# Optimization experiments

Measured on AMD Instinct MI355X. Metric: run time of the kernel, lower is better.

Reference implementation:

```python
import jax, jax.numpy as jnp
import numpy as np

NHEAD = 8
LAYER_NAMES = ('self', 'cross', 'self', 'cross')
EPS = 1e-6


def ln(x, g, b, eps=1e-5):
    m = jnp.mean(x, -1, keepdims=True)
    v = jnp.mean((x - m) ** 2, -1, keepdims=True)
    return (x - m) * jax.lax.rsqrt(v + eps) * g + b


def linear_attention(q, k, v, q_mask, kv_mask):
    # q: [N, L, H, D], k/v: [N, S, H, D]; LoFTR LinearAttention (elu+1 feature map)
    Q = jax.nn.elu(q) + 1.0
    K = jax.nn.elu(k) + 1.0
    if q_mask is not None:
        Q = Q * q_mask[:, :, None, None].astype(Q.dtype)
    if kv_mask is not None:
        mk = kv_mask[:, :, None, None].astype(K.dtype)
        K = K * mk
        v = v * mk
    v_len = v.shape[1]
    v = v / v_len
    KV = jnp.einsum('nshd,nshv->nhdv', K, v)
    Z = 1.0 / (jnp.einsum('nlhd,nhd->nlh', Q, K.sum(1)) + EPS)
    return jnp.einsum('nlhd,nhdv,nlh->nlhv', Q, KV, Z) * v_len


def enc_layer(x, src, q_mask, kv_mask, Wq, Wk, Wv, Wm, W1, W2, g1, b1, g2, b2):
    # x: [N, L, C], src: [N, S, C]
    N, L, C = x.shape
    S = src.shape[1]
    H, D = NHEAD, C // NHEAD
    q = (x @ Wq).reshape(N, L, H, D)
    k = (src @ Wk).reshape(N, S, H, D)
    v = (src @ Wv).reshape(N, S, H, D)
    msg = linear_attention(q, k, v, q_mask, kv_mask).reshape(N, L, C)
    msg = ln(msg @ Wm, g1, b1)
    msg = ln(jnp.tanh(jnp.concatenate([x, msg], axis=-1) @ W1) @ W2, g2, b2)
    return x + msg


def sample_descriptors(kp, fmap, s):
    # kp: [B, L, K, 2] (x, y) raw-image pixel coords; fmap: [B, C, H, W]; s: stride
    B, C, H, W = fmap.shape
    k = kp - s / 2 + 0.5
    denom = jnp.array([W * s - s / 2 - 0.5, H * s - s / 2 - 0.5], dtype=kp.dtype)
    k = (k / denom) * 2.0 - 1.0  # normalized [-1, 1]
    px = (k[..., 0] + 1.0) * 0.5 * (W - 1)  # align_corners=True grid_sample
    py = (k[..., 1] + 1.0) * 0.5 * (H - 1)
    x0 = jnp.floor(px)
    y0 = jnp.floor(py)
    wx = (px - x0)[..., None]
    wy = (py - y0)[..., None]
    x0i = jnp.clip(x0, 0, W - 1).astype(jnp.int32)
    x1i = jnp.clip(x0 + 1, 0, W - 1).astype(jnp.int32)
    y0i = jnp.clip(y0, 0, H - 1).astype(jnp.int32)
    y1i = jnp.clip(y0 + 1, 0, H - 1).astype(jnp.int32)
    fm = jnp.transpose(fmap, (0, 2, 3, 1))  # [B, H, W, C]
    bidx = jnp.arange(B)[:, None, None]
    g00 = fm[bidx, y0i, x0i]
    g01 = fm[bidx, y0i, x1i]
    g10 = fm[bidx, y1i, x0i]
    g11 = fm[bidx, y1i, x1i]
    out = (1 - wy) * ((1 - wx) * g00 + wx * g01) + wy * ((1 - wx) * g10 + wx * g11)
    # SuperPoint-style L2 normalization of sampled descriptors
    out = out / (jnp.linalg.norm(out, axis=-1, keepdims=True) + 1e-8)
    return out  # [B, L, K, C]


def geo_transformer(feat0, feat1, kp0_cross, kp1_cross, mask_self0, mask_self1,
                    mask_cross0, mask_cross1, Wq, Wk, Wv, Wm, W1, W2, g1, b1, g2, b2,
                    h0, w0, h1, w1, scale):
    B, L0, C = feat0.shape
    L1 = feat1.shape[1]
    K = kp0_cross.shape[2]
    for i, name in enumerate(LAYER_NAMES):
        p = (Wq[i], Wk[i], Wv[i], Wm[i], W1[i], W2[i], g1[i], b1[i], g2[i], b2[i])
        if name == 'self':
            # source = masked subset of x == full source with kv-mask (v_length cancels)
            feat0 = enc_layer(feat0, feat0, None, mask_self0, *p)
            feat1 = enc_layer(feat1, feat1, None, mask_self1, *p)
        else:
            fmap0 = jnp.transpose(feat0.reshape(B, h0, w0, C), (0, 3, 1, 2))
            fmap1 = jnp.transpose(feat1.reshape(B, h1, w1, C), (0, 3, 1, 2))
            f0c = sample_descriptors(kp0_cross, fmap0, scale)  # [B, L1, K, C]
            f1c = sample_descriptors(kp1_cross, fmap1, scale)  # [B, L0, K, C]
            x0 = feat0.reshape(B * L0, 1, C)
            x1 = feat1.reshape(B * L1, 1, C)
            nf0 = enc_layer(x0, f1c.reshape(B * L0, K, C), None,
                            mask_cross1.reshape(B * L0, K), *p)
            nf1 = enc_layer(x1, f0c.reshape(B * L1, K, C), None,
                            mask_cross0.reshape(B * L1, K), *p)
            feat0 = nf0.reshape(B, L0, C)
            feat1 = nf1.reshape(B, L1, C)
    return feat0, feat1


def setup_inputs() -> dict:
    key = jax.random.key(0)
    B, H0, W0, C, K, S, NL = 2, 64, 64, 256, 9, 8, 4
    L = H0 * W0
    ks = jax.random.split(key, 16)
    std = (2.0 / (C + C)) ** 0.5
    std2 = (2.0 / (2 * C + 2 * C)) ** 0.5
    std3 = (2.0 / (2 * C + C)) ** 0.5
    kp0 = jnp.stack([
        jax.random.uniform(ks[2], (B, L, K)) * (W0 * S),
        jax.random.uniform(ks[3], (B, L, K)) * (H0 * S)], axis=-1)
    kp1 = jnp.stack([
        jax.random.uniform(ks[4], (B, L, K)) * (W0 * S),
        jax.random.uniform(ks[5], (B, L, K)) * (H0 * S)], axis=-1)
    return {
        'feat0': jax.random.normal(ks[0], (B, L, C), jnp.float32),
        'feat1': jax.random.normal(ks[1], (B, L, C), jnp.float32),
        'kp0_cross': kp0.astype(jnp.float32),
        'kp1_cross': kp1.astype(jnp.float32),
        'mask_self0': jax.random.bernoulli(ks[6], 0.9, (B, L)),
        'mask_self1': jax.random.bernoulli(ks[7], 0.9, (B, L)),
        'mask_cross0': jax.random.bernoulli(ks[8], 0.8, (B, L, K)),
        'mask_cross1': jax.random.bernoulli(ks[9], 0.8, (B, L, K)),
        'Wq': jax.random.normal(ks[10], (NL, C, C), jnp.float32) * std,
        'Wk': jax.random.normal(ks[11], (NL, C, C), jnp.float32) * std,
        'Wv': jax.random.normal(ks[12], (NL, C, C), jnp.float32) * std,
        'Wm': jax.random.normal(ks[13], (NL, C, C), jnp.float32) * std,
        'W1': jax.random.normal(ks[14], (NL, 2 * C, 2 * C), jnp.float32) * std2,
        'W2': jax.random.normal(ks[15], (NL, 2 * C, C), jnp.float32) * std3,
        'g1': jnp.ones((NL, C), jnp.float32),
        'b1': jnp.zeros((NL, C), jnp.float32),
        'g2': jnp.ones((NL, C), jnp.float32),
        'b2': jnp.zeros((NL, C), jnp.float32),
        'h0': H0, 'w0': W0, 'h1': H0, 'w1': W0, 'scale': S,
    }


def reference(feat0, feat1, kp0_cross, kp1_cross, mask_self0, mask_self1,
              mask_cross0, mask_cross1, Wq, Wk, Wv, Wm, W1, W2, g1, b1, g2, b2,
              h0, w0, h1, w1, scale):
    return geo_transformer(feat0, feat1, kp0_cross, kp1_cross, mask_self0, mask_self1,
                           mask_cross0, mask_cross1, Wq, Wk, Wv, Wm, W1, W2,
                           g1, b1, g2, b2, h0, w0, h1, w1, scale)
```

## Files before the change

kernel.cpp:

```cpp
#include <hip/hip_runtime.h>
#include <cstddef>


#define NROWS 16384

typedef unsigned short ushort_t;
typedef __attribute__((ext_vector_type(8))) short short8;
typedef __attribute__((ext_vector_type(4))) float f32x4;
typedef __attribute__((ext_vector_type(4))) unsigned short ushort4_t;
typedef __attribute__((ext_vector_type(8))) unsigned short ushort8_t;

__device__ __forceinline__ float b2f(unsigned short u) {
    union { unsigned int i; float f; } v; v.i = (unsigned int)u << 16; return v.f;
}
__device__ __forceinline__ unsigned short f2b(float x) {
    union { float f; unsigned int i; } v; v.f = x;
    unsigned int r = v.i + 0x7fffu + ((v.i >> 16) & 1u);
    return (unsigned short)(r >> 16);
}
__device__ __forceinline__ float elu1(float x) {
    return x > 0.f ? x + 1.f : __expf(x);
}

#define ASYNC_COPY16(gptr, lptr) \
    __builtin_amdgcn_global_load_lds((const __attribute__((address_space(1))) void*)(gptr), \
                                     (__attribute__((address_space(3))) void*)(lptr), 16, 0, 0)

__global__ __launch_bounds__(256) void gemm_bf16_kernel(
    const ushort_t* __restrict__ A0, int lda0,
    const ushort_t* __restrict__ Wt, int ldw,
    ushort_t* __restrict__ C, int ldc, int Kd,
    float* __restrict__ zbuf, int znf4)
{
    __shared__ ushort_t As[128 * 64];
    __shared__ ushort_t Bs[128 * 64];

    int tid = threadIdx.x;
    int m0 = blockIdx.y * 128;
    int n0 = blockIdx.x * 128;
    int lane = tid & 63, w = tid >> 6;
    int wrow = w >> 1, wcol = w & 1;
    int quad = lane >> 4, l16 = lane & 15;

    if (zbuf && blockIdx.y == 0) {
        int nblk = gridDim.x;
        for (int i = blockIdx.x * 256 + tid; i < znf4; i += nblk * 256)
            *(float4*)&zbuf[(size_t)i * 4] = (float4){0.f, 0.f, 0.f, 0.f};
    }

    f32x4 acc[4][4];
    #pragma unroll
    for (int i = 0; i < 4; i++)
        #pragma unroll
        for (int j = 0; j < 4; j++) acc[i][j] = (f32x4){0.f, 0.f, 0.f, 0.f};

    for (int kb = 0; kb < Kd; kb += 64) {
        #pragma unroll
        for (int q = 0; q < 4; q++) {
            int s = q * 256 + tid;
            int kk = s >> 9, p = s & 511;
            int row = p >> 2, c4 = p & 3;
            ASYNC_COPY16(A0 + (size_t)(m0 + row) * lda0 + kb + kk * 32 + c4 * 8,
                         (char*)As + s * 16);
        }
        #pragma unroll
        for (int q = 0; q < 4; q++) {
            int s = q * 256 + tid;
            int kk = s >> 9, p = s & 511;
            int row = p >> 2, c4 = p & 3;
            ASYNC_COPY16(Wt + (size_t)(n0 + row) * ldw + kb + kk * 32 + c4 * 8,
                         (char*)Bs + s * 16);
        }
        __syncthreads();

        #pragma unroll
        for (int kk = 0; kk < 2; kk++) {
            short8 af[4], bf[4];
            #pragma unroll
            for (int mt = 0; mt < 4; mt++)
                af[mt] = *(const short8*)&As[kk * 4096 + (wrow * 64 + mt * 16 + l16) * 32 + quad * 8];
            #pragma unroll
            for (int nt = 0; nt < 4; nt++)
                bf[nt] = *(const short8*)&Bs[kk * 4096 + (wcol * 64 + nt * 16 + l16) * 32 + quad * 8];
            #pragma unroll
            for (int mt = 0; mt < 4; mt++)
                #pragma unroll
                for (int nt = 0; nt < 4; nt++)
                    acc[mt][nt] = __builtin_amdgcn_mfma_f32_16x16x32_bf16(
                        af[mt], bf[nt], acc[mt][nt], 0, 0, 0);
        }
        __syncthreads();
    }

    #pragma unroll
    for (int mt = 0; mt < 4; mt++) {
        int row = m0 + wrow * 64 + mt * 16 + quad * 4;
        #pragma unroll
        for (int nt = 0; nt < 4; nt++) {
            int col = n0 + wcol * 64 + nt * 16 + l16;
            #pragma unroll
            for (int r = 0; r < 4; r++)
                C[(size_t)(row + r) * ldc + col] = f2b(acc[mt][nt][r]);
        }
    }
}

__global__ __launch_bounds__(256) void gemm_ln_kernel(
    const ushort_t* __restrict__ A, int lda,
    const ushort_t* __restrict__ Wt, int ldw, int Kd,
    const float* __restrict__ g, const float* __restrict__ bp,
    ushort_t* __restrict__ OutBf)
{
    __shared__ ushort_t As[32 * 64];
    __shared__ ushort_t Bs[256 * 64];
    __shared__ float rsum[4][32];
    __shared__ float rsq[4][32];

    int tid = threadIdx.x;
    int m0 = blockIdx.x * 32;
    int lane = tid & 63, w = tid >> 6;
    int quad = lane >> 4, l16 = lane & 15;

    f32x4 acc[2][4];
    #pragma unroll
    for (int i = 0; i < 2; i++)
        #pragma unroll
        for (int j = 0; j < 4; j++) acc[i][j] = (f32x4){0.f, 0.f, 0.f, 0.f};

    for (int kb = 0; kb < Kd; kb += 64) {
        {
            int s = tid;
            int kk = s >> 7, p = s & 127;
            int row = p >> 2, c4 = p & 3;
            ASYNC_COPY16(A + (size_t)(m0 + row) * lda + kb + kk * 32 + c4 * 8,
                         (char*)As + s * 16);
        }
        #pragma unroll
        for (int q = 0; q < 8; q++) {
            int s = q * 256 + tid;
            int kk = s >> 10, p = s & 1023;
            int row = p >> 2, c4 = p & 3;
            ASYNC_COPY16(Wt + (size_t)(row) * ldw + kb + kk * 32 + c4 * 8,
                         (char*)Bs + s * 16);
        }
        __syncthreads();

        #pragma unroll
        for (int kk = 0; kk < 2; kk++) {
            short8 af[2], bf[4];
            #pragma unroll
            for (int mt = 0; mt < 2; mt++)
                af[mt] = *(const short8*)&As[kk * 1024 + (mt * 16 + l16) * 32 + quad * 8];
            #pragma unroll
            for (int nt = 0; nt < 4; nt++)
                bf[nt] = *(const short8*)&Bs[kk * 8192 + (w * 64 + nt * 16 + l16) * 32 + quad * 8];
            #pragma unroll
            for (int mt = 0; mt < 2; mt++)
                #pragma unroll
                for (int nt = 0; nt < 4; nt++)
                    acc[mt][nt] = __builtin_amdgcn_mfma_f32_16x16x32_bf16(
                        af[mt], bf[nt], acc[mt][nt], 0, 0, 0);
        }
        __syncthreads();
    }

    #pragma unroll
    for (int mt = 0; mt < 2; mt++)
        #pragma unroll
        for (int r = 0; r < 4; r++) {
            float s = 0.f, q = 0.f;
            #pragma unroll
            for (int nt = 0; nt < 4; nt++) {
                float v = acc[mt][nt][r];
                s += v; q += v * v;
            }
            #pragma unroll
            for (int off = 1; off < 16; off <<= 1) {
                s += __shfl_xor(s, off, 64);
                q += __shfl_xor(q, off, 64);
            }
            if (l16 == 0) {
                rsum[w][mt * 16 + quad * 4 + r] = s;
                rsq[w][mt * 16 + quad * 4 + r]  = q;
            }
        }
    __syncthreads();

    #pragma unroll
    for (int mt = 0; mt < 2; mt++) {
        #pragma unroll
        for (int r = 0; r < 4; r++) {
            int rl = mt * 16 + quad * 4 + r;
            float s = rsum[0][rl] + rsum[1][rl] + rsum[2][rl] + rsum[3][rl];
            float q = rsq[0][rl] + rsq[1][rl] + rsq[2][rl] + rsq[3][rl];
            float m = s * (1.f / 256.f);
            float var = q * (1.f / 256.f) - m * m;
            float rs = rsqrtf(var + 1e-5f);
            size_t row = (size_t)(m0 + rl);
            #pragma unroll
            for (int nt = 0; nt < 4; nt++) {
                int col = w * 64 + nt * 16 + l16;
                float y = (acc[mt][nt][r] - m) * rs * g[col] + bp[col];
                OutBf[row * 256 + col] = f2b(y);
            }
        }
    }
}

__global__ __launch_bounds__(256) void mlp_fused_kernel(
    const ushort_t* __restrict__ Xb, const ushort_t* __restrict__ L1,
    const ushort_t* __restrict__ W1t, const ushort_t* __restrict__ W2t,
    const float* __restrict__ g, const float* __restrict__ bp,
    ushort_t* __restrict__ XbfOut, const float* __restrict__ Xin,
    float* __restrict__ Xout)
{
    __shared__ ushort_t Tt[32 * 512];
    __shared__ char buf[20480];

    ushort_t* As  = (ushort_t*)buf;
    ushort_t* Bs  = (ushort_t*)(buf + 4096);
    ushort_t* Bs2 = (ushort_t*)buf;
    float* rsum = (float*)buf;
    float* rsq  = (float*)(buf + 512);

    int tid = threadIdx.x;
    int m0 = blockIdx.x * 32;
    int lane = tid & 63, w = tid >> 6;
    int quad = lane >> 4, l16 = lane & 15;

    for (int np = 0; np < 4; np++) {
        f32x4 acc[2][2];
        #pragma unroll
        for (int i = 0; i < 2; i++)
            #pragma unroll
            for (int j = 0; j < 2; j++) acc[i][j] = (f32x4){0.f, 0.f, 0.f, 0.f};

        for (int kb = 0; kb < 512; kb += 64) {
            const ushort_t* Ab = (kb < 256) ? Xb : L1;
            int kc = (kb < 256) ? kb : kb - 256;
            {
                int s = tid;
                int kk = s >> 7, p = s & 127;
                ASYNC_COPY16(Ab + (size_t)(m0 + (p >> 2)) * 256 + kc + kk * 32 + (p & 3) * 8,
                             (char*)As + s * 16);
            }
            #pragma unroll
            for (int q = 0; q < 4; q++) {
                int s = q * 256 + tid;
                int kk = s >> 9, p = s & 511;
                ASYNC_COPY16(W1t + (size_t)(np * 128 + (p >> 2)) * 512 + kb + kk * 32 + (p & 3) * 8,
                             (char*)Bs + s * 16);
            }
            __syncthreads();

            #pragma unroll
            for (int kk = 0; kk < 2; kk++) {
                short8 af[2], bfr[2];
                #pragma unroll
                for (int mt = 0; mt < 2; mt++)
                    af[mt] = *(const short8*)&As[kk * 1024 + (mt * 16 + l16) * 32 + quad * 8];
                #pragma unroll
                for (int nt = 0; nt < 2; nt++)
                    bfr[nt] = *(const short8*)&Bs[kk * 4096 + (w * 32 + nt * 16 + l16) * 32 + quad * 8];
                #pragma unroll
                for (int mt = 0; mt < 2; mt++)
                    #pragma unroll
                    for (int nt = 0; nt < 2; nt++)
                        acc[mt][nt] = __builtin_amdgcn_mfma_f32_16x16x32_bf16(
                            af[mt], bfr[nt], acc[mt][nt], 0, 0, 0);
            }
            __syncthreads();
        }

        #pragma unroll
        for (int mt = 0; mt < 2; mt++)
            #pragma unroll
            for (int nt = 0; nt < 2; nt++)
                #pragma unroll
                for (int r = 0; r < 4; r++) {
                    int trow = mt * 16 + quad * 4 + r;
                    int col = np * 128 + w * 32 + nt * 16 + l16;
                    int c8s = (col >> 3) ^ (trow & 7);
                    Tt[trow * 512 + c8s * 8 + (col & 7)] = f2b(tanhf(acc[mt][nt][r]));
                }
    }

    f32x4 acc2[2][2][2];
    #pragma unroll
    for (int a = 0; a < 2; a++)
        #pragma unroll
        for (int i = 0; i < 2; i++)
            #pragma unroll
            for (int j = 0; j < 2; j++) acc2[a][i][j] = (f32x4){0.f, 0.f, 0.f, 0.f};

    for (int pass = 0; pass < 2; pass++) {
        for (int kb = 0; kb < 512; kb += 64) {
            #pragma unroll
            for (int q = 0; q < 4; q++) {
                int s = q * 256 + tid;
                int kk = s >> 9, p = s & 511;
                ASYNC_COPY16(W2t + (size_t)(pass * 128 + (p >> 2)) * 512 + kb + kk * 32 + (p & 3) * 8,
                             (char*)Bs2 + s * 16);
            }
            __syncthreads();

            #pragma unroll
            for (int kk = 0; kk < 2; kk++) {
                short8 af[2], bfr[2];
                #pragma unroll
                for (int mt = 0; mt < 2; mt++) {
                    int row = mt * 16 + l16;
                    int blk = ((kb >> 3) + kk * 4 + quad) ^ (row & 7);
                    af[mt] = *(const short8*)&Tt[row * 512 + blk * 8];
                }
                #pragma unroll
                for (int nt = 0; nt < 2; nt++)
                    bfr[nt] = *(const short8*)&Bs2[kk * 4096 + (w * 32 + nt * 16 + l16) * 32 + quad * 8];
                #pragma unroll
                for (int mt = 0; mt < 2; mt++)
                    #pragma unroll
                    for (int nt = 0; nt < 2; nt++)
                        acc2[pass][mt][nt] = __builtin_amdgcn_mfma_f32_16x16x32_bf16(
                            af[mt], bfr[nt], acc2[pass][mt][nt], 0, 0, 0);
            }
            __syncthreads();
        }
    }

    #pragma unroll
    for (int mt = 0; mt < 2; mt++)
        #pragma unroll
        for (int r = 0; r < 4; r++) {
            float s = 0.f, q = 0.f;
            #pragma unroll
            for (int pass = 0; pass < 2; pass++)
                #pragma unroll
                for (int nt = 0; nt < 2; nt++) {
                    float v = acc2[pass][mt][nt][r];
                    s += v; q += v * v;
                }
            #pragma unroll
            for (int off = 1; off < 16; off <<= 1) {
                s += __shfl_xor(s, off, 64);
                q += __shfl_xor(q, off, 64);
            }
            if (l16 == 0) {
                rsum[w * 32 + mt * 16 + quad * 4 + r] = s;
                rsq[w * 32 + mt * 16 + quad * 4 + r]  = q;
            }
        }
    __syncthreads();

    #pragma unroll
    for (int mt = 0; mt < 2; mt++) {
        #pragma unroll
        for (int r = 0; r < 4; r++) {
            int rl = mt * 16 + quad * 4 + r;
            float s = rsum[rl] + rsum[32 + rl] + rsum[64 + rl] + rsum[96 + rl];
            float q = rsq[rl] + rsq[32 + rl] + rsq[64 + rl] + rsq[96 + rl];
            float m = s * (1.f / 256.f);
            float var = q * (1.f / 256.f) - m * m;
            float rs = rsqrtf(var + 1e-5f);
            size_t row = (size_t)(m0 + rl);
            #pragma unroll
            for (int pass = 0; pass < 2; pass++)
                #pragma unroll
                for (int nt = 0; nt < 2; nt++) {
                    int col = pass * 128 + w * 32 + nt * 16 + l16;
                    float y = (acc2[pass][mt][nt][r] - m) * rs * g[col] + bp[col];
                    float xn = Xin[row * 256 + col] + y;
                    Xout[row * 256 + col] = xn;
                    XbfOut[row * 256 + col] = f2b(xn);
                }
        }
    }
}

__global__ __launch_bounds__(256) void wprep_kernel(
    const float* __restrict__ Wq, const float* __restrict__ Wk,
    const float* __restrict__ Wv, const float* __restrict__ Wm,
    const float* __restrict__ W1, const float* __restrict__ W2,
    ushort_t* __restrict__ Wqkvt, ushort_t* __restrict__ Wmt,
    ushort_t* __restrict__ W1t, ushort_t* __restrict__ W2t)
{
    int t = blockIdx.x;
    int layer = t / 640, r = t % 640;
    const float* src; ushort_t* dst;
    int ldsrc, lddst, tn, tk;
    if (r < 192) {
        int grp = r / 64, rr = r % 64; tn = rr / 8; tk = rr % 8;
        src = (grp == 0 ? Wq : grp == 1 ? Wk : Wv) + (size_t)layer * 65536;
        ldsrc = 256;
        dst = Wqkvt + (size_t)layer * 196608 + (size_t)grp * 65536;
        lddst = 256;
    } else if (r < 256) {
        int rr = r - 192; tn = rr / 8; tk = rr % 8;
        src = Wm + (size_t)layer * 65536; ldsrc = 256;
        dst = Wmt + (size_t)layer * 65536; lddst = 256;
    } else if (r < 512) {
        int rr = r - 256; tn = rr / 16; tk = rr % 16;
        src = W1 + (size_t)layer * 262144; ldsrc = 512;
        dst = W1t + (size_t)layer * 262144; lddst = 512;
    } else {
        int rr = r - 512; tn = rr / 16; tk = rr % 16;
        src = W2 + (size_t)layer * 131072; ldsrc = 256;
        dst = W2t + (size_t)layer * 131072; lddst = 512;
    }
    int n0 = tn * 32, k0 = tk * 32;
    __shared__ float tileS[32][33];
    int j = threadIdx.x & 31, i0 = threadIdx.x >> 5;
    #pragma unroll
    for (int p = 0; p < 4; p++) {
        int i = i0 + p * 8;
        tileS[i][j] = src[(size_t)(k0 + i) * ldsrc + n0 + j];
    }
    __syncthreads();
    #pragma unroll
    for (int p = 0; p < 4; p++) {
        int i = i0 + p * 8;
        dst[(size_t)(n0 + i) * lddst + k0 + j] = f2b(tileS[j][i]);
    }
}

__global__ __launch_bounds__(256) void init_kernel(
    const float* __restrict__ f0, const float* __restrict__ f1,
    float* __restrict__ X, ushort_t* __restrict__ Xbf)
{
    int idx = blockIdx.x * 256 + threadIdx.x;
    size_t e = (size_t)idx * 4;
    float4 v = (e < 2097152) ? *(const float4*)&f0[e] : *(const float4*)&f1[e - 2097152];
    *(float4*)&X[e] = v;
    ushort4_t u = { f2b(v.x), f2b(v.y), f2b(v.z), f2b(v.w) };
    *(ushort4_t*)&Xbf[e] = u;
}

__global__ __launch_bounds__(256) void kv_reduce_kernel(
    const ushort_t* __restrict__ QKV,
    const int* __restrict__ mask0, const int* __restrict__ mask1,
    float* __restrict__ KV, float* __restrict__ Ksum)
{
    int g = blockIdx.y;
    int t = g >> 4, b = (g >> 3) & 1, h = g & 7;
    const int* mask = t ? mask1 : mask0;
    int rowbase = t * 8192 + b * 4096;
    int s_begin = blockIdx.x * 256;

    __shared__ float sK[32][32];
    __shared__ float sV[32][32];

    int tid = threadIdx.x;
    int e  = tid & 31;
    int dq = tid >> 5;

    float acc[4] = {0.f, 0.f, 0.f, 0.f};
    float ks[4]  = {0.f, 0.f, 0.f, 0.f};

    for (int s0 = s_begin; s0 < s_begin + 256; s0 += 32) {
        #pragma unroll
        for (int q = 0; q < 2; q++) {
            int idx = tid + q * 256;
            int rl = idx >> 4;
            int part = idx & 15;
            int s = s0 + rl;
            size_t row = (size_t)(rowbase + s);
            float m = mask[b * 4096 + s] ? 1.f : 0.f;
            if (part < 8) {
                ushort4_t u = *(const ushort4_t*)&QKV[row * 768 + 256 + h * 32 + part * 4];
                float4 f = { elu1(b2f(u.x)) * m, elu1(b2f(u.y)) * m,
                             elu1(b2f(u.z)) * m, elu1(b2f(u.w)) * m };
                *(float4*)&sK[rl][part * 4] = f;
            } else {
                ushort4_t u = *(const ushort4_t*)&QKV[row * 768 + 512 + h * 32 + (part - 8) * 4];
                float4 f = { b2f(u.x) * m, b2f(u.y) * m, b2f(u.z) * m, b2f(u.w) * m };
                *(float4*)&sV[rl][(part - 8) * 4] = f;
            }
        }
        __syncthreads();

        #pragma unroll
        for (int s = 0; s < 32; s++) {
            float4 kq = *(const float4*)&sK[s][dq * 4];
            float vv = sV[s][e];
            acc[0] += kq.x * vv;
            acc[1] += kq.y * vv;
            acc[2] += kq.z * vv;
            acc[3] += kq.w * vv;
            ks[0] += kq.x; ks[1] += kq.y; ks[2] += kq.z; ks[3] += kq.w;
        }
        __syncthreads();
    }

    #pragma unroll
    for (int j = 0; j < 4; j++)
        atomicAdd(&KV[(size_t)g * 1024 + (dq * 4 + j) * 32 + e], acc[j]);
    if (e == 0) {
        #pragma unroll
        for (int j = 0; j < 4; j++)
            atomicAdd(&Ksum[g * 32 + dq * 4 + j], ks[j]);
    }
}

__global__ __launch_bounds__(256) void attn_apply_kernel(
    const ushort_t* __restrict__ QKV, const float* __restrict__ KV,
    const float* __restrict__ Ksum, ushort_t* __restrict__ MSG)
{
    int row = blockIdx.x;
    int t = row >> 13, bb = (row >> 12) & 1;
    int gb = (t * 2 + bb) * 8;
    int c = threadIdx.x, h = c >> 5, e = c & 31;
    int g = gb + h;

    __shared__ float sQ[256];
    float qf = elu1(b2f(QKV[(size_t)row * 768 + c]));
    sQ[c] = qf;
    __syncthreads();

    float p = qf * Ksum[g * 32 + e];
    #pragma unroll
    for (int off = 16; off; off >>= 1) p += __shfl_xor(p, off, 32);
    float Z = 1.f / (p + 1e-6f);

    float acc = 0.f;
    #pragma unroll
    for (int d = 0; d < 32; d++)
        acc += sQ[h * 32 + d] * KV[(size_t)g * 1024 + d * 32 + e];

    MSG[(size_t)row * 256 + c] = f2b(acc * Z);
}

__global__ __launch_bounds__(256) void gram_kernel(
    const ushort_t* __restrict__ Xbf, float* __restrict__ Gm)
{
    int a = blockIdx.x * 4 + (threadIdx.x >> 6);
    int lane = threadIdx.x & 63;
    int img = a / 4225;
    int rr = a - img * 4225;
    int ay = rr / 65, ax = rr - ay * 65;
    int xa = ax > 0 ? ax - 1 : 0;
    int xb = ax < 64 ? ax : 63;
    if (ax == 0) xb = 0;
    int ya = ay > 0 ? ay - 1 : 0;
    int yb = ay < 64 ? ay : 63;
    if (ay == 0) yb = 0;

    size_t rbase = (size_t)img * 4096;
    size_t r0 = (rbase + ya * 64 + xa) * 256;
    size_t r1 = (rbase + ya * 64 + xb) * 256;
    size_t r2 = (rbase + yb * 64 + xa) * 256;
    size_t r3 = (rbase + yb * 64 + xb) * 256;

    int c4 = lane * 4;
    ushort4_t u0 = *(const ushort4_t*)&Xbf[r0 + c4];
    ushort4_t u1 = *(const ushort4_t*)&Xbf[r1 + c4];
    ushort4_t u2 = *(const ushort4_t*)&Xbf[r2 + c4];
    ushort4_t u3 = *(const ushort4_t*)&Xbf[r3 + c4];

    float p[10] = {0,0,0,0,0,0,0,0,0,0};
    #pragma unroll
    for (int j = 0; j < 4; j++) {
        float f0 = b2f(u0[j]), f1 = b2f(u1[j]), f2 = b2f(u2[j]), f3 = b2f(u3[j]);
        p[0] += f0 * f0; p[1] += f0 * f1; p[2] += f0 * f2; p[3] += f0 * f3;
        p[4] += f1 * f1; p[5] += f1 * f2; p[6] += f1 * f3;
        p[7] += f2 * f2; p[8] += f2 * f3; p[9] += f3 * f3;
    }
    #pragma unroll
    for (int k = 0; k < 10; k++)
        #pragma unroll
        for (int off = 32; off; off >>= 1) p[k] += __shfl_xor(p[k], off, 64);

    if (lane == 0) {
        #pragma unroll
        for (int k = 0; k < 10; k++) Gm[(size_t)a * 12 + k] = p[k];
    }
}

__global__ __launch_bounds__(256) void cross_fused_kernel(
    const ushort_t* __restrict__ QKV, const float* __restrict__ Gm,
    const float* __restrict__ kp0, const float* __restrict__ kp1,
    const int* __restrict__ maskc0, const int* __restrict__ maskc1,
    ushort_t* __restrict__ MSG)
{
    int wv = threadIdx.x >> 6;
    int lane = threadIdx.x & 63;
    int half = lane >> 5;
    int l32 = lane & 31;

    int blk = blockIdx.x;
    int qd = (blk & 7) >> 1;
    int within = ((blk >> 3) << 1) | (blk & 1);
    int row = qd * 4096 + within * 4 + wv;

    int t = row >> 13;
    int bl = row & 8191;
    int ts = 1 - t;
    const float* kp = ts ? kp1 : kp0;
    const int* mask = (t == 0) ? maskc1 : maskc0;
    int img = ts * 2 + (bl >> 12);
    int rb = img * 4096;
    const float* Gimg = Gm + (size_t)img * 50700;

    int c8 = l32 * 8;

    ushort8_t qu = *(const ushort8_t*)&QKV[(size_t)row * 768 + c8];
    float qf[8];
    #pragma unroll
    for (int j = 0; j < 8; j++) qf[j] = elu1(b2f(qu[j]));

    int sbase[5], sdx[5], sdy[5];
    float su0[5], su1[5], su2[5], su3[5], sm[5];
    #pragma unroll
    for (int si = 0; si < 5; si++) {
        int s9 = half + 2 * si;
        int valid = (s9 < 9);
        int r = bl * 9 + (valid ? s9 : 0);
        sm[si] = (valid && mask[r] != 0) ? 1.f : 0.f;

        float2 xy = *(const float2*)&kp[(size_t)r * 2];
        float px = (xy.x - 3.5f) * (63.f / 507.5f);
        float py = (xy.y - 3.5f) * (63.f / 507.5f);
        float fx = floorf(px), fy = floorf(py);
        float wx = px - fx, wy = py - fy;
        int ix = (int)fx, iy = (int)fy;
        int xa = ix > 0 ? ix : 0;
        int xb = ix + 1 > 0 ? (ix + 1 < 63 ? ix + 1 : 63) : 0;
        int ya = iy > 0 ? iy : 0;
        int yb = iy + 1 > 0 ? (iy + 1 < 63 ? iy + 1 : 63) : 0;

        float w0 = (1.f - wy) * (1.f - wx);
        float w1 = (1.f - wy) * wx;
        float w2 = wy * (1.f - wx);
        float w3 = wy * wx;

        const float* G = &Gimg[(size_t)((iy + 1) * 65 + (ix + 1)) * 12];
        float4 ga = *(const float4*)&G[0];
        float4 gb4 = *(const float4*)&G[4];
        float2 gc = *(const float2*)&G[8];
        float ss = w0 * w0 * ga.x + w1 * w1 * gb4.x + w2 * w2 * gb4.w + w3 * w3 * gc.y
                 + 2.f * (w0 * w1 * ga.y + w0 * w2 * ga.z + w0 * w3 * ga.w
                        + w1 * w2 * gb4.y + w1 * w3 * gb4.z + w2 * w3 * gc.x);
        float inv = 1.f / (sqrtf(ss) + 1e-8f);
        su0[si] = w0 * inv; su1[si] = w1 * inv;
        su2[si] = w2 * inv; su3[si] = w3 * inv;

        sbase[si] = (rb + ya * 64 + xa) * 768;
        sdx[si] = (xb - xa) * 768;
        sdy[si] = (yb - ya) * 49152;
    }

    ushort8_t kR[2][4], vR[2][4];

#define LOADKV(bufi, si_) do { \
        size_t bK = (size_t)sbase[si_] + 256 + c8; \
        size_t bV = (size_t)sbase[si_] + 512 + c8; \
        int dx = sdx[si_], dy = sdy[si_]; \
        kR[bufi][0] = *(const ushort8_t*)&QKV[bK]; \
        kR[bufi][1] = *(const ushort8_t*)&QKV[bK + dx]; \
        kR[bufi][2] = *(const ushort8_t*)&QKV[bK + dy]; \
        kR[bufi][3] = *(const ushort8_t*)&QKV[bK + dx + dy]; \
        vR[bufi][0] = *(const ushort8_t*)&QKV[bV]; \
        vR[bufi][1] = *(const ushort8_t*)&QKV[bV + dx]; \
        vR[bufi][2] = *(const ushort8_t*)&QKV[bV + dy]; \
        vR[bufi][3] = *(const ushort8_t*)&QKV[bV + dx + dy]; \
    } while (0)

    float zsum = 0.f;
    float acc[8] = {0, 0, 0, 0, 0, 0, 0, 0};

    LOADKV(0, 0);
    #pragma unroll
    for (int si = 0; si < 5; si++) {
        int cur = si & 1;
        if (si + 1 < 5) {
            if (cur == 0) LOADKV(1, si + 1);
            else          LOADKV(0, si + 1);
        }
        float u0 = su0[si], u1 = su1[si], u2 = su2[si], u3 = su3[si];
        float vc[8];
        float p = 0.f;
        #pragma unroll
        for (int j = 0; j < 8; j++) {
            float kc = u0 * b2f(kR[cur][0][j]) + u1 * b2f(kR[cur][1][j])
                     + u2 * b2f(kR[cur][2][j]) + u3 * b2f(kR[cur][3][j]);
            vc[j] = u0 * b2f(vR[cur][0][j]) + u1 * b2f(vR[cur][1][j])
                  + u2 * b2f(vR[cur][2][j]) + u3 * b2f(vR[cur][3][j]);
            p += qf[j] * elu1(kc);
        }
        p += __shfl_xor(p, 1, 64);
        p += __shfl_xor(p, 2, 64);
        p *= sm[si];

        zsum += p;
        #pragma unroll
        for (int j = 0; j < 8; j++) acc[j] += p * vc[j];
    }
#undef LOADKV

    zsum += __shfl_xor(zsum, 32, 64);
    #pragma unroll
    for (int j = 0; j < 8; j++) acc[j] += __shfl_xor(acc[j], 32, 64);

    if (half == 0) {
        float Z = 1.f / (zsum + 1e-6f);
        ushort8_t o;
        #pragma unroll
        for (int j = 0; j < 8; j++) o[j] = f2b(acc[j] * Z);
        *(ushort8_t*)&MSG[(size_t)row * 256 + c8] = o;
    }
}


extern "C" void kernel_launch(void* const* d_in, const int* in_sizes, int n_in,
                              void* d_out, int out_size, void* d_ws, size_t ws_size,
                              hipStream_t stream)
{
    const float* feat0 = (const float*)d_in[0];
    const float* feat1 = (const float*)d_in[1];
    const float* kp0 = (const float*)d_in[2];
    const float* kp1 = (const float*)d_in[3];
    const int* ms0 = (const int*)d_in[4];
    const int* ms1 = (const int*)d_in[5];
    const int* mc0 = (const int*)d_in[6];
    const int* mc1 = (const int*)d_in[7];
    const float* Wq = (const float*)d_in[8];
    const float* Wk = (const float*)d_in[9];
    const float* Wv = (const float*)d_in[10];
    const float* Wm = (const float*)d_in[11];
    const float* W1 = (const float*)d_in[12];
    const float* W2 = (const float*)d_in[13];
    const float* g1 = (const float*)d_in[14];
    const float* b1 = (const float*)d_in[15];
    const float* g2 = (const float*)d_in[16];
    const float* b2 = (const float*)d_in[17];

    char* p = (char*)d_ws;
    float*    X     = (float*)p;            p += 16777216;
    ushort_t* Xbf   = (ushort_t*)p;         p += 8388608;
    ushort_t* QKV   = (ushort_t*)p;         p += 25165824;
    ushort_t* MSG   = (ushort_t*)p;         p += 8388608;
    ushort_t* L1bf  = (ushort_t*)p;         p += 8388608;
    float*    KVb   = (float*)p;            p += 131072;
    float*    KSb   = (float*)p;            p += 4096;
    float*    Gm    = (float*)p;            p += 811264;
    ushort_t* Wqkvt = (ushort_t*)p;         p += 1572864;
    ushort_t* Wmt   = (ushort_t*)p;         p += 524288;
    ushort_t* W1t   = (ushort_t*)p;         p += 2097152;
    ushort_t* W2t   = (ushort_t*)p;         p += 1048576;

    init_kernel<<<4096, 256, 0, stream>>>(feat0, feat1, X, Xbf);
    wprep_kernel<<<2560, 256, 0, stream>>>(Wq, Wk, Wv, Wm, W1, W2, Wqkvt, Wmt, W1t, W2t);

    for (int i = 0; i < 4; i++) {
        const ushort_t* Wqkvt_l = Wqkvt + (size_t)i * 196608;
        const ushort_t* Wmt_l   = Wmt   + (size_t)i * 65536;
        const ushort_t* W1t_l   = W1t   + (size_t)i * 262144;
        const ushort_t* W2t_l   = W2t   + (size_t)i * 131072;
        const float* g1_l = g1 + (size_t)i * 256;
        const float* b1_l = b1 + (size_t)i * 256;
        const float* g2_l = g2 + (size_t)i * 256;
        const float* b2_l = b2 + (size_t)i * 256;
        bool is_self = (i == 0 || i == 2);

        gemm_bf16_kernel<<<dim3(6, 128), 256, 0, stream>>>(
            Xbf, 256, Wqkvt_l, 256, QKV, 768, 256,
            is_self ? KVb : nullptr, 33792 / 4);

        if (is_self) {
            kv_reduce_kernel<<<dim3(16, 32), 256, 0, stream>>>(QKV, ms0, ms1, KVb, KSb);
            attn_apply_kernel<<<NROWS, 256, 0, stream>>>(QKV, KVb, KSb, MSG);
        } else {
            gram_kernel<<<4225, 256, 0, stream>>>(Xbf, Gm);
            cross_fused_kernel<<<NROWS / 4, 256, 0, stream>>>(QKV, Gm, kp0, kp1, mc0, mc1, MSG);
        }

        gemm_ln_kernel<<<NROWS / 32, 256, 0, stream>>>(
            MSG, 256, Wmt_l, 256, 256, g1_l, b1_l, L1bf);

        float* Xout = (i == 3) ? (float*)d_out : X;
        mlp_fused_kernel<<<NROWS / 32, 256, 0, stream>>>(
            Xbf, L1bf, W1t_l, W2t_l, g2_l, b2_l, Xbf, X, Xout);
    }
}
```

Before: 617.5 us.

## Store QKV in fp16 and share sample setup across lanes in cross attention

The QKV GEMM output is now written as fp16 instead of bf16, and the consumers read it with native half-to-float conversion. In the sampled cross-attention kernel, each lane computes the bilinear weights and addresses for a single sample, and the results are broadcast with shuffles instead of every lane recomputing all five samples. The sample offsets are packed into one int, and the V interpolation is folded into the accumulation. This cuts redundant per-lane ALU and register use, but fp16 narrows the representable range of the QKV values, and any other consumers still decoding bf16 (not visible here) would become inconsistent.

```diff
diff --git a/kernel.cpp b/kernel.cpp
--- a/kernel.cpp
+++ b/kernel.cpp
@@ -9,6 +9,9 @@
 typedef __attribute__((ext_vector_type(4))) float f32x4;
 typedef __attribute__((ext_vector_type(4))) unsigned short ushort4_t;
 typedef __attribute__((ext_vector_type(8))) unsigned short ushort8_t;
+typedef _Float16 half_t;
+typedef __attribute__((ext_vector_type(4))) _Float16 half4;
+typedef __attribute__((ext_vector_type(8))) _Float16 half8;
 
 __device__ __forceinline__ float b2f(unsigned short u) {
     union { unsigned int i; float f; } v; v.i = (unsigned int)u << 16; return v.f;
@@ -17,6 +20,9 @@
     union { float f; unsigned int i; } v; v.f = x;
     unsigned int r = v.i + 0x7fffu + ((v.i >> 16) & 1u);
     return (unsigned short)(r >> 16);
+}
+__device__ __forceinline__ ushort_t f2h(float x) {
+    union { half_t h; ushort_t u; } v; v.h = (half_t)x; return v.u;
 }
 __device__ __forceinline__ float elu1(float x) {
     return x > 0.f ? x + 1.f : __expf(x);
@@ -100,7 +106,7 @@
             int col = n0 + wcol * 64 + nt * 16 + l16;
             #pragma unroll
             for (int r = 0; r < 4; r++)
-                C[(size_t)(row + r) * ldc + col] = f2b(acc[mt][nt][r]);
+                C[(size_t)(row + r) * ldc + col] = f2h(acc[mt][nt][r]);
         }
     }
 }
@@ -465,13 +471,14 @@
             size_t row = (size_t)(rowbase + s);
             float m = mask[b * 4096 + s] ? 1.f : 0.f;
             if (part < 8) {
-                ushort4_t u = *(const ushort4_t*)&QKV[row * 768 + 256 + h * 32 + part * 4];
-                float4 f = { elu1(b2f(u.x)) * m, elu1(b2f(u.y)) * m,
-                             elu1(b2f(u.z)) * m, elu1(b2f(u.w)) * m };
+                half4 u = *(const half4*)&QKV[row * 768 + 256 + h * 32 + part * 4];
+                float4 f = { elu1((float)u[0]) * m, elu1((float)u[1]) * m,
+                             elu1((float)u[2]) * m, elu1((float)u[3]) * m };
                 *(float4*)&sK[rl][part * 4] = f;
             } else {
-                ushort4_t u = *(const ushort4_t*)&QKV[row * 768 + 512 + h * 32 + (part - 8) * 4];
-                float4 f = { b2f(u.x) * m, b2f(u.y) * m, b2f(u.z) * m, b2f(u.w) * m };
+                half4 u = *(const half4*)&QKV[row * 768 + 512 + h * 32 + (part - 8) * 4];
+                float4 f = { (float)u[0] * m, (float)u[1] * m,
+                             (float)u[2] * m, (float)u[3] * m };
                 *(float4*)&sV[rl][(part - 8) * 4] = f;
             }
         }
@@ -511,7 +518,7 @@
     int g = gb + h;
 
     __shared__ float sQ[256];
-    float qf = elu1(b2f(QKV[(size_t)row * 768 + c]));
+    float qf = elu1((float)(*(const half_t*)&QKV[(size_t)row * 768 + c]));
     sQ[c] = qf;
     __syncthreads();
 
@@ -601,19 +608,19 @@
 
     int c8 = l32 * 8;
 
-    ushort8_t qu = *(const ushort8_t*)&QKV[(size_t)row * 768 + c8];
+    half8 qu = *(const half8*)&QKV[(size_t)row * 768 + c8];
     float qf[8];
     #pragma unroll
-    for (int j = 0; j < 8; j++) qf[j] = elu1(b2f(qu[j]));
-
-    int sbase[5], sdx[5], sdy[5];
-    float su0[5], su1[5], su2[5], su3[5], sm[5];
-    #pragma unroll
-    for (int si = 0; si < 5; si++) {
-        int s9 = half + 2 * si;
+    for (int j = 0; j < 8; j++) qf[j] = elu1((float)qu[j]);
+
+    float mU0, mU1, mU2, mU3, mSm;
+    int mPack;
+    {
+        int msi = l32 % 5;
+        int s9 = half + 2 * msi;
         int valid = (s9 < 9);
         int r = bl * 9 + (valid ? s9 : 0);
-        sm[si] = (valid && mask[r] != 0) ? 1.f : 0.f;
+        mSm = (valid && mask[r] != 0) ? 1.f : 0.f;
 
         float2 xy = *(const float2*)&kp[(size_t)r * 2];
         float px = (xy.x - 3.5f) * (63.f / 507.5f);
@@ -639,28 +646,42 @@
                  + 2.f * (w0 * w1 * ga.y + w0 * w2 * ga.z + w0 * w3 * ga.w
                         + w1 * w2 * gb4.y + w1 * w3 * gb4.z + w2 * w3 * gc.x);
         float inv = 1.f / (sqrtf(ss) + 1e-8f);
-        su0[si] = w0 * inv; su1[si] = w1 * inv;
-        su2[si] = w2 * inv; su3[si] = w3 * inv;
-
-        sbase[si] = (rb + ya * 64 + xa) * 768;
-        sdx[si] = (xb - xa) * 768;
-        sdy[si] = (yb - ya) * 49152;
-    }
-
-    ushort8_t kR[2][4], vR[2][4];
+        mU0 = w0 * inv; mU1 = w1 * inv; mU2 = w2 * inv; mU3 = w3 * inv;
+
+        int base = (rb + ya * 64 + xa) * 768;
+        mPack = base | (xb - xa) | ((yb - ya) << 1);
+    }
+
+    int spack[5];
+    float su0[5], su1[5], su2[5], su3[5], sm[5];
+    int srcb = half * 32;
+    #pragma unroll
+    for (int si = 0; si < 5; si++) {
+        int src = srcb + si;
+        spack[si] = __shfl(mPack, src, 64);
+        su0[si] = __shfl(mU0, src, 64);
+        su1[si] = __shfl(mU1, src, 64);
+        su2[si] = __shfl(mU2, src, 64);
+        su3[si] = __shfl(mU3, src, 64);
+        sm[si]  = __shfl(mSm, src, 64);
+    }
+
+    half8 kR[2][4], vR[2][4];
 
 #define LOADKV(bufi, si_) do { \
-        size_t bK = (size_t)sbase[si_] + 256 + c8; \
-        size_t bV = (size_t)sbase[si_] + 512 + c8; \
-        int dx = sdx[si_], dy = sdy[si_]; \
-        kR[bufi][0] = *(const ushort8_t*)&QKV[bK]; \
-        kR[bufi][1] = *(const ushort8_t*)&QKV[bK + dx]; \
-        kR[bufi][2] = *(const ushort8_t*)&QKV[bK + dy]; \
-        kR[bufi][3] = *(const ushort8_t*)&QKV[bK + dx + dy]; \
-        vR[bufi][0] = *(const ushort8_t*)&QKV[bV]; \
-        vR[bufi][1] = *(const ushort8_t*)&QKV[bV + dx]; \
-        vR[bufi][2] = *(const ushort8_t*)&QKV[bV + dy]; \
-        vR[bufi][3] = *(const ushort8_t*)&QKV[bV + dx + dy]; \
+        int pk = spack[si_]; \
+        int dx = (pk & 1) ? 768 : 0; \
+        int dy = (pk & 2) ? 49152 : 0; \
+        size_t bK = (size_t)(pk & ~3) + 256 + c8; \
+        size_t bV = bK + 256; \
+        kR[bufi][0] = *(const half8*)&QKV[bK]; \
+        kR[bufi][1] = *(const half8*)&QKV[bK + dx]; \
+        kR[bufi][2] = *(const half8*)&QKV[bK + dy]; \
+        kR[bufi][3] = *(const half8*)&QKV[bK + dx + dy]; \
+        vR[bufi][0] = *(const half8*)&QKV[bV]; \
+        vR[bufi][1] = *(const half8*)&QKV[bV + dx]; \
+        vR[bufi][2] = *(const half8*)&QKV[bV + dy]; \
+        vR[bufi][3] = *(const half8*)&QKV[bV + dx + dy]; \
     } while (0)
 
     float zsum = 0.f;
@@ -675,14 +696,11 @@
             else          LOADKV(0, si + 1);
         }
         float u0 = su0[si], u1 = su1[si], u2 = su2[si], u3 = su3[si];
-        float vc[8];
         float p = 0.f;
         #pragma unroll
         for (int j = 0; j < 8; j++) {
-            float kc = u0 * b2f(kR[cur][0][j]) + u1 * b2f(kR[cur][1][j])
-                     + u2 * b2f(kR[cur][2][j]) + u3 * b2f(kR[cur][3][j]);
-            vc[j] = u0 * b2f(vR[cur][0][j]) + u1 * b2f(vR[cur][1][j])
-                  + u2 * b2f(vR[cur][2][j]) + u3 * b2f(vR[cur][3][j]);
+            float kc = u0 * (float)kR[cur][0][j] + u1 * (float)kR[cur][1][j]
+                     + u2 * (float)kR[cur][2][j] + u3 * (float)kR[cur][3][j];
             p += qf[j] * elu1(kc);
         }
         p += __shfl_xor(p, 1, 64);
@@ -690,8 +708,11 @@
         p *= sm[si];
 
         zsum += p;
-        #pragma unroll
-        for (int j = 0; j < 8; j++) acc[j] += p * vc[j];
+        float pu0 = p * u0, pu1 = p * u1, pu2 = p * u2, pu3 = p * u3;
+        #pragma unroll
+        for (int j = 0; j < 8; j++)
+            acc[j] += pu0 * (float)vR[cur][0][j] + pu1 * (float)vR[cur][1][j]
+                    + pu2 * (float)vR[cur][2][j] + pu3 * (float)vR[cur][3][j];
     }
 #undef LOADKV
 
```

New measurement: 597.0 us. 3.3% less time.
